# Kernel optimization log

Measured on AMD Instinct MI355X. Metric: run time of the kernel, lower is better.

Reference implementation:

```python
import jax, jax.numpy as jnp
import numpy as np
from jax import lax

T, B = 32, 16
NUM_ACTIONS = 18
HID = 256
C_V, C_K, C_S, NQ = 120, 8, 64, 4
NKEY, NVAL = C_K + C_S, C_V + C_S
Hh, Ww = 27, 20


def _spatial_basis():
    # Fourier spatial basis from Mott et al.; U = V = 8 -> 64 channels.
    h, w, U = Hh, Ww, 8
    p_h = np.arange(1, h + 1)[:, None] * np.ones((1, w)) * (np.pi / h)
    p_w = np.ones((h, 1)) * np.arange(1, w + 1)[None, :] * (np.pi / w)
    u = np.arange(1, U + 1)
    a = np.cos(p_h[:, :, None] * u)  # (h,w,8)
    b = np.cos(p_w[:, :, None] * u)  # (h,w,8)
    S = np.einsum('hwu,hwv->hwuv', a, b).reshape(h, w, U * U)
    return jnp.asarray(S, jnp.float32)

_S = _spatial_basis()


def _conv(x, w, b, stride, pad):
    y = lax.conv_general_dilated(x, w, stride, pad,
                                 dimension_numbers=('NCHW', 'OIHW', 'NCHW'))
    return y + b[None, :, None, None]


def setup_inputs() -> dict:
    key = jax.random.key(0)
    ks = iter(jax.random.split(key, 40))
    f32 = jnp.float32
    def rn(shape, s=0.05):
        return jax.random.normal(next(ks), shape, dtype=f32) * s
    return dict(
        frame=jax.random.normal(next(ks), (T, B, 3, 210, 160), dtype=f32),
        done=jnp.zeros((T, B), dtype=bool),
        last_action=jax.random.randint(next(ks), (T, B), 0, NUM_ACTIONS),
        reward=jax.random.normal(next(ks), (T, B), dtype=f32),
        core_h=jnp.zeros((B, HID), f32), core_c=jnp.zeros((B, HID), f32),
        conv_h=jnp.zeros((B, HID // 2, Hh, Ww), f32),
        conv_c=jnp.zeros((B, HID // 2, Hh, Ww), f32),
        cnn_w1=rn((32, 3, 8, 8)), cnn_b1=rn((32,)),
        cnn_w2=rn((64, 32, 4, 4)), cnn_b2=rn((64,)),
        lstm_w=rn((512, 192, 3, 3)), lstm_b=rn((512,)),
        qw1=rn((HID, 128)), qb1=rn((128,)),
        qw2=rn((128, NQ * NKEY)), qb2=rn((NQ * NKEY,)),
        qw3=rn((NQ * NKEY, NQ * NKEY)), qb3=rn((NQ * NKEY,)),
        aw1=rn((NVAL * NQ + NKEY * NQ + 1 + NUM_ACTIONS, 2 * HID)), ab1=rn((2 * HID,)),
        aw2=rn((2 * HID, HID)), ab2=rn((HID,)),
        w_ih=rn((4 * HID, HID)), w_hh=rn((4 * HID, HID)),
        b_ih=rn((4 * HID,)), b_hh=rn((4 * HID,)),
        pw=rn((HID, NUM_ACTIONS)), pb=rn((NUM_ACTIONS,)),
        vw=rn((HID, 1)), vb=rn((1,)),
    )


def reference(frame, done, last_action, reward, core_h, core_c, conv_h, conv_c,
              cnn_w1, cnn_b1, cnn_w2, cnn_b2, lstm_w, lstm_b,
              qw1, qb1, qw2, qb2, qw3, qb3, aw1, ab1, aw2, ab2,
              w_ih, w_hh, b_ih, b_hh, pw, pb, vw, vb):
    x = frame.reshape(T * B, 3, 210, 160)
    x = _conv(x, cnn_w1, cnn_b1, (4, 4), [(1, 1), (2, 2)])
    x = _conv(x, cnn_w2, cnn_b2, (2, 2), [(2, 2), (1, 1)])  # (T*B,64,27,20)
    x = x.reshape(T, B, 64, Hh, Ww)
    nd = (~done).astype(jnp.float32)  # (T,B)

    def vis_step(carry, inp):
        h, c = carry
        x_t, nd_t = inp
        m = nd_t[:, None, None, None]
        h, c = m * h, m * c
        gates = _conv(jnp.concatenate([x_t, h], axis=1), lstm_w, lstm_b,
                      (1, 1), [(1, 1), (1, 1)])
        ai, af, ao, ag = jnp.split(gates, 4, axis=1)
        c = jax.nn.sigmoid(af) * c + jax.nn.sigmoid(ai) * jnp.tanh(ag)
        h = jax.nn.sigmoid(ao) * jnp.tanh(c)
        return (h, c), h

    (vh, vc), O = lax.scan(vis_step, (conv_h, conv_c), (x, nd))
    # Faithful to the original `.view(N, h, w, c)` (a reinterpret, not a transpose).
    O = O.reshape(T * B, Hh, Ww, 128)
    Sb = jnp.broadcast_to(_S, (T * B, Hh, Ww, C_S))
    K = jnp.concatenate([O[..., :C_K], Sb], axis=3).reshape(T, B, Hh, Ww, NKEY)
    V = jnp.concatenate([O[..., C_K:], Sb], axis=3).reshape(T, B, Hh, Ww, NVAL)

    a1h = jax.nn.one_hot(last_action, NUM_ACTIONS, dtype=jnp.float32)  # (T,B,A)
    r = jnp.clip(reward, -1.0, 1.0)[..., None]  # (T,B,1)

    def core_step(carry, inp):
        h, c = carry
        K_t, V_t, r_t, a_t, nd_t = inp
        q = jax.nn.relu(h @ qw1 + qb1)
        q = jax.nn.relu(q @ qw2 + qb2)
        q = (q @ qw3 + qb3).reshape(B, NQ, NKEY)
        A = jnp.einsum('bhwk,bqk->bhwq', K_t, q)
        A = jax.nn.softmax(A.reshape(B, Hh * Ww, NQ), axis=1).reshape(B, Hh, Ww, NQ)
        ans = jnp.einsum('bhwq,bhwv->bqv', A, V_t)  # (B,NQ,NVAL)
        answer = jnp.concatenate(
            [ans.reshape(B, -1), q.reshape(B, -1), r_t, a_t], axis=1)
        ci = jax.nn.relu(answer @ aw1 + ab1) @ aw2 + ab2
        m = nd_t[:, None]
        h, c = m * h, m * c
        gates = ci @ w_ih.T + b_ih + h @ w_hh.T + b_hh  # torch gate order i,f,g,o
        gi, gf, gg, go = jnp.split(gates, 4, axis=1)
        c = jax.nn.sigmoid(gf) * c + jax.nn.sigmoid(gi) * jnp.tanh(gg)
        h = jax.nn.sigmoid(go) * jnp.tanh(c)
        return (h, c), h

    (ch, cc), outs = lax.scan(core_step, (core_h, core_c), (K, V, r, a1h, nd))
    out = outs.reshape(T * B, HID)
    logits = out @ pw + pb
    values = out @ vw + vb
    action = jnp.argmax(logits, axis=1)  # eval-mode action selection
    return (logits.reshape(T, B, NUM_ACTIONS), values.reshape(T, B),
            action.reshape(T, B), ch, cc, vh, vc)
```

## Files before the change

### kernel.cpp

```cpp
#include <hip/hip_runtime.h>
#include <math.h>

#define T_ 32
#define B_ 16
#define NA 18
#define P_ 540

typedef __attribute__((ext_vector_type(8)))  short short8;
typedef __attribute__((ext_vector_type(16))) float f32x16;

__device__ __forceinline__ float sigm(float x){ return 1.0f/(1.0f+expf(-x)); }
__device__ __forceinline__ unsigned short f2bf(float f){
    unsigned u = __float_as_uint(f);
    u += 0x7fff + ((u>>16)&1u);
    return (unsigned short)(u>>16);
}
__device__ __forceinline__ float bfu(unsigned short u){ return __uint_as_float(((unsigned)u)<<16); }

__global__ __launch_bounds__(256) void conv1k(const float* __restrict__ frame,
                                              const float* __restrict__ w,
                                              const float* __restrict__ bias,
                                              unsigned short* __restrict__ c1pad){
    __shared__ float tile[6048];
    int bid = blockIdx.x;
    int n = bid / 26, oh = (bid % 26)*2;
    int tid = threadIdx.x;
    const float* fb = frame + (size_t)n*3*210*160;
    for (int s = tid; s < 6048; s += 256){
        int col = s % 168;
        int row = (s/168) % 12;
        int ic  = s / 2016;
        int iy = oh*4 - 1 + row;
        int ix = col - 2;
        float v = 0.f;
        if (iy >= 0 && iy < 210 && ix >= 0 && ix < 160) v = fb[ic*33600 + iy*160 + ix];
        tile[s] = v;
    }
    __syncthreads();
    int oc = tid & 31, grp = tid >> 5;
    float acc[10] = {0.f,0.f,0.f,0.f,0.f,0.f,0.f,0.f,0.f,0.f};
    const float* wb = w + oc*192;
    for (int ic=0; ic<3; ++ic){
        #pragma unroll
        for (int kh=0; kh<8; ++kh){
            const float* wr = wb + ic*64 + kh*8;
            float4 w0 = *((const float4*)wr);
            float4 w1 = *((const float4*)(wr+4));
            const float* rowA = tile + ic*2016 + kh*168 + grp*20;
            float r[24];
            *((float4*)(r+ 0)) = *((const float4*)(rowA+ 0));
            *((float4*)(r+ 4)) = *((const float4*)(rowA+ 4));
            *((float4*)(r+ 8)) = *((const float4*)(rowA+ 8));
            *((float4*)(r+12)) = *((const float4*)(rowA+12));
            *((float4*)(r+16)) = *((const float4*)(rowA+16));
            *((float4*)(r+20)) = *((const float4*)(rowA+20));
            #pragma unroll
            for (int o=0;o<5;++o){
                acc[o] += r[o*4+0]*w0.x + r[o*4+1]*w0.y + r[o*4+2]*w0.z + r[o*4+3]*w0.w
                        + r[o*4+4]*w1.x + r[o*4+5]*w1.y + r[o*4+6]*w1.z + r[o*4+7]*w1.w;
            }
            const float* rowB = rowA + 672;
            *((float4*)(r+ 0)) = *((const float4*)(rowB+ 0));
            *((float4*)(r+ 4)) = *((const float4*)(rowB+ 4));
            *((float4*)(r+ 8)) = *((const float4*)(rowB+ 8));
            *((float4*)(r+12)) = *((const float4*)(rowB+12));
            *((float4*)(r+16)) = *((const float4*)(rowB+16));
            *((float4*)(r+20)) = *((const float4*)(rowB+20));
            #pragma unroll
            for (int o=0;o<5;++o){
                acc[5+o] += r[o*4+0]*w0.x + r[o*4+1]*w0.y + r[o*4+2]*w0.z + r[o*4+3]*w0.w
                          + r[o*4+4]*w1.x + r[o*4+5]*w1.y + r[o*4+6]*w1.z + r[o*4+7]*w1.w;
            }
        }
    }
    float bi = bias[oc];
    unsigned short* ob = c1pad + ((size_t)(n*32 + oc)*56 + oh+2)*42 + 1;
    #pragma unroll
    for (int o=0;o<5;++o) ob[grp*5+o] = f2bf(acc[o] + bi);
    ob += 42;
    #pragma unroll
    for (int o=0;o<5;++o) ob[grp*5+o] = f2bf(acc[5+o] + bi);
}

__global__ void apack2k(const float* __restrict__ w2, unsigned short* __restrict__ ap){
    int idx = blockIdx.x*256 + threadIdx.x;
    if (idx >= 32768) return;
    int j = idx & 7;
    int lane = (idx>>3) & 63;
    int mt = (idx>>9) & 1;
    int ic = idx >> 10;
    int k = ((lane>>5)<<3) + j;
    int oc = mt*32 + (lane & 31);
    ap[idx] = f2bf(w2[((oc*32 + ic)<<4) + k]);
}

__global__ __launch_bounds__(256) void c2mfma(const unsigned short* __restrict__ c1pad,
                                              const unsigned short* __restrict__ apack2,
                                              const float* __restrict__ bias,
                                              unsigned short* __restrict__ xre){
    __shared__ unsigned short p2[2][3072];
    __shared__ float bsm[64];
    int bid = blockIdx.x;
    int s = bid / 5;
    int n0 = (bid % 5) * 128;
    int tid = threadIdx.x;
    int wave = tid >> 6, lane = tid & 63;
    int khalf = (lane>>5) << 3;
    if (tid < 64) bsm[tid] = bias[tid];
    const unsigned short* cb = c1pad + (size_t)s*32*2352;

    int soff[8], swaddr[8];
    #pragma unroll
    for (int q=0;q<8;++q){
        int idx = q*256 + tid;
        int n = idx & 127, k = idx >> 7;
        int p = n0 + n; if (p > 539) p = 539;
        soff[q] = ((p/20)*2 + (k>>2))*42 + (p%20)*2 + (k&3);
        swaddr[q] = n*24 + k;
    }
    #pragma unroll
    for (int q=0;q<8;++q) p2[0][swaddr[q]] = cb[soff[q]];
    unsigned short rv[8];
    #pragma unroll
    for (int q=0;q<8;++q) rv[q] = cb[2352 + soff[q]];

    int mt = wave >> 1, ntb = (wave & 1) * 2;
    short8 acur = *((const short8*)(apack2 + ((size_t)mt*64 + lane)*8));
    short8 anxt;
    f32x16 acc[2];
    #pragma unroll
    for (int jj=0;jj<2;++jj)
        #pragma unroll
        for (int rg=0;rg<16;++rg) acc[jj][rg] = 0.f;
    __syncthreads();

    for (int c=0; c<32; ++c){
        int buf = c & 1;
        if (c < 31){
            #pragma unroll
            for (int q=0;q<8;++q) p2[buf^1][swaddr[q]] = rv[q];
        }
        if (c < 30){
            const unsigned short* src = cb + (size_t)(c+2)*2352;
            #pragma unroll
            for (int q=0;q<8;++q) rv[q] = src[soff[q]];
        }
        if (c < 31) anxt = *((const short8*)(apack2 + ((size_t)((c+1)*2 + mt)*64 + lane)*8));
        #pragma unroll
        for (int jj=0;jj<2;++jj){
            int n = (ntb+jj)*32 + (lane & 31);
            short8 bf = *((const short8*)(&p2[buf][n*24 + khalf]));
            acc[jj] = __builtin_amdgcn_mfma_f32_32x32x16_bf16(acur, bf, acc[jj], 0, 0, 0);
        }
        acur = anxt;
        __syncthreads();
    }
    #pragma unroll
    for (int jj=0;jj<2;++jj){
        int pos = n0 + (ntb+jj)*32 + (lane & 31);
        if (pos >= 540) continue;
        unsigned short* op = xre + ((size_t)s*540 + pos)*64;
        #pragma unroll
        for (int rg=0; rg<16; ++rg){
            int oc = mt*32 + (rg & 3) + 8*(rg>>2) + 4*(lane>>5);
            op[oc] = f2bf(acc[jj][rg] + bsm[oc]);
        }
    }
}

__global__ void sbasisk(float* __restrict__ S){
    int idx = blockIdx.x*256 + threadIdx.x;
    if (idx >= P_*64) return;
    int s = idx & 63, p = idx >> 6;
    int y = p/20, x = p%20;
    int u = s >> 3, v = s & 7;
    double a  = cos((double)((y+1)*(u+1)) * M_PI / 27.0);
    double bb = cos((double)((x+1)*(v+1)) * M_PI / 20.0);
    S[idx] = (float)(a*bb);
}

__global__ void packw4k(const float* __restrict__ in, unsigned short* __restrict__ out, int R, int C){
    int idx = blockIdx.x*256 + threadIdx.x;
    int r4cnt = (R+3)>>2;
    if (idx >= r4cnt*C*4) return;
    int j = idx & 3;
    int rc = idx >> 2;
    int c = rc % C;
    int r = (rc / C)*4 + j;
    out[idx] = (r < R) ? f2bf(in[(size_t)r*C + c]) : (unsigned short)0;
}
__global__ void packt4k(const float* __restrict__ in, unsigned short* __restrict__ out, int R, int C){
    int idx = blockIdx.x*256 + threadIdx.x;
    int r4cnt = (R+3)>>2;
    if (idx >= r4cnt*C*4) return;
    int j = idx & 3;
    int rc = idx >> 2;
    int c = rc % C;
    int r = (rc / C)*4 + j;
    out[idx] = (r < R) ? f2bf(in[(size_t)c*R + r]) : (unsigned short)0;
}

__global__ void apack9k(const float* __restrict__ lw, unsigned short* __restrict__ ap){
    int idx = blockIdx.x*256 + threadIdx.x;
    if (idx >= 884736) return;
    int j = idx & 7;
    int lane = (idx>>3) & 63;
    int mt = (idx>>9) & 15;
    int f  = idx >> 13;
    int tap = f / 12, c = f % 12;
    int ch = c*16 + ((lane>>5)<<3) + j;
    int oc = mt*32 + (lane & 31);
    ap[idx] = f2bf(lw[(size_t)oc*1728 + ch*9 + tap]);
}

__global__ void h0rek(const float* __restrict__ h0, unsigned short* __restrict__ h0re){
    int idx = blockIdx.x*256 + threadIdx.x;
    if (idx >= 16*128*540) return;
    int plane = idx / 540, p = idx % 540;
    int b = plane >> 7, c = plane & 127;
    h0re[((size_t)b*540 + p)*128 + c] = f2bf(h0[idx]);
}

__global__ __launch_bounds__(512) void gvck(const unsigned short* __restrict__ xre,
                                            const unsigned short* __restrict__ hrd,
                                            unsigned short* __restrict__ hwr,
                                            const unsigned short* __restrict__ h0re,
                                            const unsigned short* __restrict__ apack,
                                            const float* __restrict__ lb,
                                            const unsigned char* __restrict__ done,
                                            float* __restrict__ vh, float* __restrict__ vc,
                                            unsigned short* __restrict__ hreA,
                                            const float* __restrict__ S,
                                            const unsigned short* __restrict__ pq1, const float* __restrict__ qb1,
                                            const unsigned short* __restrict__ pq2, const float* __restrict__ qb2,
                                            const unsigned short* __restrict__ pq3, const float* __restrict__ qb3,
                                            const unsigned short* __restrict__ pa1, const float* __restrict__ ab1,
                                            const unsigned short* __restrict__ pa2, const float* __restrict__ ab2,
                                            const unsigned short* __restrict__ pih, const unsigned short* __restrict__ phh,
                                            const float* __restrict__ bih, const float* __restrict__ bhh,
                                            const float* __restrict__ reward, const int* __restrict__ lact,
                                            float* __restrict__ hsb, float* __restrict__ csb,
                                            float* __restrict__ outs,
                                            int t){
    __shared__ __align__(16) unsigned char smraw[65536];
    int bid = blockIdx.x;
    int tid = threadIdx.x;

    if (bid >= 16){
        if (t >= T_) return;
        float* gsm = (float*)smraw;
        int vb = bid - 16;
        int b  = vb % 16;
        int r  = vb / 16;
        int nb = r % 9;
        int mh = r / 9;
        int wave = tid >> 6, lane = tid & 63;
        int khalf = (lane>>5) << 3;
        int n0 = nb * 64;
        bool dn = done[t*B_ + b];

        const unsigned short* xb = xre + (size_t)(t*B_ + b)*540*64;
        const unsigned short* hp2 = (t==0) ? (h0re + (size_t)b*540*128)
                                           : (hrd  + (size_t)b*540*128);

        int mt = (wave>>1)*4 + mh*2 + (wave&1);

        int poff[2][9]; int vmask[2][9];
        #pragma unroll
        for (int jj=0;jj<2;++jj){
            int p = n0 + jj*32 + (lane & 31); if (p > 539) p = 539;
            int y = p/20, x = p%20;
            #pragma unroll
            for (int tap=0;tap<9;++tap){
                int dy = tap/3 - 1, dx = tap%3 - 1;
                int yy = y+dy, xx = x+dx;
                vmask[jj][tap] = ((unsigned)yy < 27u) && ((unsigned)xx < 20u);
                poff[jj][tap] = yy*20 + xx;
            }
        }
// ... 66 lines not shown
                    int pos = (flat/2560)*20 + (flat/128)%20;
                    int ch  = flat & 127;
                    hreA[((size_t)(t*B_ + b)*540 + pos)*128 + ch] = hb16;
                }
            }
        }
        return;
    }

    if (t == 0) return;
    int tc = t - 1;
    int b = bid;
    float* fs = (float*)smraw;
    float* hs   = fs;
    float* cs   = fs + 256;
    float* hs2  = fs + 512;
    float* q1   = fs + 768;
    float* q2   = fs + 896;
    float* q3   = fs + 1184;
    float* elog = fs + 1472;
    float* red  = fs + 3632;
    float* ansv = fs + 3664;
    float* hid  = fs + 4720;
    float* cis  = fs + 5232;
    float* gb   = fs + 5488;

    if (tid < 256){ hs[tid] = hsb[b*256+tid]; cs[tid] = csb[b*256+tid]; }
    if (tid >= 256 && tid < 269) ansv[1043 + (tid-256)] = 0.f;
    __syncthreads();

    float m = done[tc*B_+b] ? 0.f : 1.f;
    if (tid < 128){
        float a0=0.f,a1=0.f,a2=0.f,a3=0.f;
        for (int i4=0;i4<64;++i4){
            ushort4 w = *((const ushort4*)(pq1 + (size_t)((i4<<7)+tid)*4));
            float4 h4 = *((const float4*)(hs + i4*4));
            a0 += h4.x*bfu(w.x); a1 += h4.y*bfu(w.y);
            a2 += h4.z*bfu(w.z); a3 += h4.w*bfu(w.w);
        }
        q1[tid] = fmaxf(qb1[tid] + ((a0+a1)+(a2+a3)), 0.f);
    }
    __syncthreads();
    if (tid < 288){
        float a0=0.f,a1=0.f,a2=0.f,a3=0.f;
        for (int i4=0;i4<32;++i4){
            ushort4 w = *((const ushort4*)(pq2 + (size_t)(i4*288+tid)*4));
            float4 h4 = *((const float4*)(q1 + i4*4));
            a0 += h4.x*bfu(w.x); a1 += h4.y*bfu(w.y);
            a2 += h4.z*bfu(w.z); a3 += h4.w*bfu(w.w);
        }
        q2[tid] = fmaxf(qb2[tid] + ((a0+a1)+(a2+a3)), 0.f);
    }
    __syncthreads();
    if (tid < 288){
        float a0=0.f,a1=0.f,a2=0.f,a3=0.f;
        for (int i4=0;i4<72;++i4){
            ushort4 w = *((const ushort4*)(pq3 + (size_t)(i4*288+tid)*4));
            float4 h4 = *((const float4*)(q2 + i4*4));
            a0 += h4.x*bfu(w.x); a1 += h4.y*bfu(w.y);
            a2 += h4.z*bfu(w.z); a3 += h4.w*bfu(w.w);
        }
        float a = qb3[tid] + ((a0+a1)+(a2+a3));
        q3[tid] = a;
        ansv[736+tid] = a;
    }
    if (tid == 0){ float r = reward[tc*B_+b]; ansv[1024] = fminf(1.f,fmaxf(-1.f,r)); }
    if (tid >= 32 && tid < 32+NA) ansv[1025 + tid-32] = (lact[tc*B_+b] == tid-32) ? 1.f : 0.f;
    __syncthreads();

    const unsigned short* hrb = hreA + (size_t)(tc*B_ + b)*540*128;
    for (int idx = tid; idx < 4*P_; idx += 512){
        int qi = idx / P_, p = idx % P_;
        const unsigned short* hp = hrb + (size_t)p*128;
        uint4 hv = *((const uint4*)hp);
        const float* qv = q3 + qi*72;
        float a = __uint_as_float(hv.x<<16)*qv[0] + __uint_as_float(hv.x & 0xffff0000u)*qv[1]
                + __uint_as_float(hv.y<<16)*qv[2] + __uint_as_float(hv.y & 0xffff0000u)*qv[3]
                + __uint_as_float(hv.z<<16)*qv[4] + __uint_as_float(hv.z & 0xffff0000u)*qv[5]
                + __uint_as_float(hv.w<<16)*qv[6] + __uint_as_float(hv.w & 0xffff0000u)*qv[7];
        const float* Sp = S + p*64;
        #pragma unroll
        for (int s2=0;s2<16;++s2){
            float4 sv = *((const float4*)(Sp + 4*s2));
            a += sv.x*qv[8+4*s2] + sv.y*qv[9+4*s2] + sv.z*qv[10+4*s2] + sv.w*qv[11+4*s2];
        }
        elog[qi*P_ + p] = a;
    }
    __syncthreads();
    {
        int qi = tid >> 7, lt = tid & 127;
        float mx = -1e30f;
        for (int p = lt; p < P_; p += 128) mx = fmaxf(mx, elog[qi*P_ + p]);
        for (int off=32; off; off>>=1) mx = fmaxf(mx, __shfl_down(mx, off));
        if ((tid & 63) == 0) red[tid>>6] = mx;
        __syncthreads();
        if (tid < 4) red[16+tid] = fmaxf(red[2*tid], red[2*tid+1]);
        __syncthreads();
        mx = red[16+qi];
        float sm = 0.f;
        for (int p = lt; p < P_; p += 128){ float e = expf(elog[qi*P_ + p]-mx); elog[qi*P_ + p] = e; sm += e; }
        for (int off=32; off; off>>=1) sm += __shfl_down(sm, off);
        if ((tid & 63) == 0) red[8 + (tid>>6)] = sm;
        __syncthreads();
        if (tid < 4) red[24+tid] = red[8+2*tid] + red[8+2*tid+1];
        __syncthreads();
    }
    if (tid < 240){
        int g = tid >> 2;
        int qi = g / 15, vb = g % 15;
        int pc = tid & 3;
        float ac[8] = {0,0,0,0,0,0,0,0};
        const unsigned short* hb8 = hrb + 8 + vb*8;
        for (int p = pc*135; p < pc*135+135; ++p){
            float e = elog[qi*P_ + p];
            uint4 hv = *((const uint4*)(hb8 + (size_t)p*128));
            ac[0] += e*__uint_as_float(hv.x<<16);
            ac[1] += e*__uint_as_float(hv.x & 0xffff0000u);
            ac[2] += e*__uint_as_float(hv.y<<16);
            ac[3] += e*__uint_as_float(hv.y & 0xffff0000u);
            ac[4] += e*__uint_as_float(hv.z<<16);
            ac[5] += e*__uint_as_float(hv.z & 0xffff0000u);
            ac[6] += e*__uint_as_float(hv.w<<16);
            ac[7] += e*__uint_as_float(hv.w & 0xffff0000u);
        }
        #pragma unroll
        for (int j=0;j<8;++j){ ac[j] += __shfl_down(ac[j],2); ac[j] += __shfl_down(ac[j],1); }
        if ((tid&3)==0){
            float inv2 = 1.f/red[24+qi];
            #pragma unroll
            for (int j=0;j<8;++j) ansv[qi*184 + vb*8 + j] = ac[j]*inv2;
        }
    } else if (tid < 496){
        int u = tid - 240;
        int g = u >> 2;
        int qi = g >> 4, vb4 = g & 15;
        int pc = u & 3;
        float ac[4] = {0,0,0,0};
        const float* Sp = S + vb4*4;
        for (int p = pc*135; p < pc*135+135; ++p){
            float e = elog[qi*P_ + p];
            float4 sv = *((const float4*)(Sp + (size_t)p*64));
            ac[0]+=e*sv.x; ac[1]+=e*sv.y; ac[2]+=e*sv.z; ac[3]+=e*sv.w;
        }
        #pragma unroll
        for (int j=0;j<4;++j){ ac[j] += __shfl_down(ac[j],2); ac[j] += __shfl_down(ac[j],1); }
        if ((tid&3)==0){
            float inv2 = 1.f/red[24+qi];
            #pragma unroll
            for (int j=0;j<4;++j) ansv[qi*184 + 120 + vb4*4 + j] = ac[j]*inv2;
        }
    }
    __syncthreads();
    {
        float a0=ab1[tid], a1=0.f, a2=0.f, a3=0.f;
        for (int i4=0;i4<261;++i4){
            ushort4 w = *((const ushort4*)(pa1 + (size_t)((i4<<9)+tid)*4));
            float4 av = *((const float4*)(ansv + i4*4));
            a0 += av.x*bfu(w.x); a1 += av.y*bfu(w.y);
            a2 += av.z*bfu(w.z); a3 += av.w*bfu(w.w);
        }
        hid[tid] = fmaxf((a0+a1)+(a2+a3), 0.f);
    }
    if (tid < 256) hs2[tid] = hs[tid]*m;
    __syncthreads();
    if (tid < 256){
        float a0=ab2[tid],a1=0.f,a2=0.f,a3=0.f;
        for (int i4=0;i4<128;++i4){
            ushort4 w = *((const ushort4*)(pa2 + (size_t)((i4<<8)+tid)*4));
            float4 hv = *((const float4*)(hid + i4*4));
            a0 += hv.x*bfu(w.x); a1 += hv.y*bfu(w.y);
            a2 += hv.z*bfu(w.z); a3 += hv.w*bfu(w.w);
        }
        cis[tid] = (a0+a1)+(a2+a3);
    }
    __syncthreads();
    for (int g = tid; g < 1024; g += 512){
        float a0=bih[g]+bhh[g], a1=0.f, a2=0.f, a3=0.f;
        for (int i4=0;i4<64;++i4){
            ushort4 wi = *((const ushort4*)(pih + (size_t)((i4<<10)+g)*4));
            ushort4 wh = *((const ushort4*)(phh + (size_t)((i4<<10)+g)*4));
            float4 cv = *((const float4*)(cis + i4*4));
            float4 hv = *((const float4*)(hs2 + i4*4));
            a0 += cv.x*bfu(wi.x) + hv.x*bfu(wh.x);
            a1 += cv.y*bfu(wi.y) + hv.y*bfu(wh.y);
            a2 += cv.z*bfu(wi.z) + hv.z*bfu(wh.z);
            a3 += cv.w*bfu(wi.w) + hv.w*bfu(wh.w);
        }
        gb[g] = (a0+a1)+(a2+a3);
    }
    __syncthreads();
    if (tid < 256){
        float gi = gb[tid], gf = gb[256+tid], gg = gb[512+tid], go = gb[768+tid];
        float cold = cs[tid]*m;
        float cn = sigm(gf)*cold + sigm(gi)*tanhf(gg);
        float hn = sigm(go)*tanhf(cn);
        csb[b*256+tid] = cn;
        hsb[b*256+tid] = hn;
        outs[(tc*B_+b)*256+tid] = hn;
    }
}

__global__ __launch_bounds__(64) void finalk(const float* __restrict__ outs,
                                             const float* __restrict__ pw, const float* __restrict__ pb,
                                             const float* __restrict__ vw, const float* __restrict__ vb,
                                             float* __restrict__ dout){
    int row = blockIdx.x, tid = threadIdx.x;
    __shared__ float os[256];
    __shared__ float lg[NA];
    for (int i=tid; i<256; i+=64) os[i] = outs[row*256+i];
    __syncthreads();
    if (tid < NA){
        float a = pb[tid];
        for (int i=0;i<256;++i) a += os[i]*pw[i*NA+tid];
        lg[tid] = a;
        dout[row*NA + tid] = a;
    } else if (tid == 32){
        float a = vb[0];
        for (int i=0;i<256;++i) a += os[i]*vw[i];
        dout[9216 + row] = a;
// ... 7 lines not shown
}

extern "C" void kernel_launch(void* const* d_in, const int* in_sizes, int n_in,
                              void* d_out, int out_size, void* d_ws, size_t ws_size,
                              hipStream_t stream) {
    const float* frame   = (const float*)d_in[0];
    const unsigned char* done = (const unsigned char*)d_in[1];
    const int*   lact    = (const int*)d_in[2];
    const float* reward  = (const float*)d_in[3];
    const float* core_h0 = (const float*)d_in[4];
    const float* core_c0 = (const float*)d_in[5];
    const float* conv_h0 = (const float*)d_in[6];
    const float* conv_c0 = (const float*)d_in[7];
    const float* cnn_w1  = (const float*)d_in[8];
    const float* cnn_b1  = (const float*)d_in[9];
    const float* cnn_w2  = (const float*)d_in[10];
    const float* cnn_b2  = (const float*)d_in[11];
    const float* lstm_w  = (const float*)d_in[12];
    const float* lstm_b  = (const float*)d_in[13];
    const float* qw1 = (const float*)d_in[14]; const float* qb1 = (const float*)d_in[15];
    const float* qw2 = (const float*)d_in[16]; const float* qb2 = (const float*)d_in[17];
    const float* qw3 = (const float*)d_in[18]; const float* qb3 = (const float*)d_in[19];
    const float* aw1 = (const float*)d_in[20]; const float* ab1 = (const float*)d_in[21];
    const float* aw2 = (const float*)d_in[22]; const float* ab2 = (const float*)d_in[23];
    const float* w_ih = (const float*)d_in[24]; const float* w_hh = (const float*)d_in[25];
    const float* b_ih = (const float*)d_in[26]; const float* b_hh = (const float*)d_in[27];
    const float* pw = (const float*)d_in[28]; const float* pb = (const float*)d_in[29];
    const float* vw = (const float*)d_in[30]; const float* vb = (const float*)d_in[31];

    float* ws = (float*)d_ws;
    float* dout = (float*)d_out;

    unsigned short* xre    = (unsigned short*)ws;
    unsigned short* c1pad  = (unsigned short*)(ws + 10485760);
    unsigned short* hreA   = (unsigned short*)(ws + 10485760);
    unsigned short* apack  = (unsigned short*)(ws + 28180480);
    unsigned short* wpk    = (unsigned short*)(ws + 28966912);
    unsigned short* pq1 = wpk;
    unsigned short* pq2 = wpk + 32768;
    unsigned short* pq3 = wpk + 69632;
    unsigned short* pa1 = wpk + 152576;
    unsigned short* pa2 = wpk + 687104;
    unsigned short* pih = wpk + 818176;
    unsigned short* phh = wpk + 1080320;
    unsigned short* h0re   = (unsigned short*)(ws + 29753344);
    unsigned short* apack2 = (unsigned short*)(ws + 30408704);
    unsigned short* hpl0   = (unsigned short*)(ws + 30425088);
    float* hsb   = ws + 31080448;
    float* csb   = ws + 31084544;
    unsigned short* hpl1   = (unsigned short*)(ws + 31100928);
    float* vh    = ws + 34881536;
    float* vc    = ws + 35987456;
    float* S     = ws + 37093376;
    float* outs  = ws + 37127936;

    hipMemsetAsync(c1pad, 0, (size_t)38535168*2, stream);

    apack2k<<<128, 256, 0, stream>>>(cnn_w2, apack2);
    conv1k<<<512*26, 256, 0, stream>>>(frame, cnn_w1, cnn_b1, c1pad);
    c2mfma<<<2560, 256, 0, stream>>>(c1pad, apack2, cnn_b2, xre);

    sbasisk<<<135, 256, 0, stream>>>(S);
    apack9k<<<3456, 256, 0, stream>>>(lstm_w, apack);
    packw4k<<<128,  256, 0, stream>>>(qw1, pq1, 256, 128);
    packw4k<<<144,  256, 0, stream>>>(qw2, pq2, 128, 288);
    packw4k<<<324,  256, 0, stream>>>(qw3, pq3, 288, 288);
    packw4k<<<2088, 256, 0, stream>>>(aw1, pa1, 1043, 512);
    packw4k<<<512,  256, 0, stream>>>(aw2, pa2, 512, 256);
    packt4k<<<1024, 256, 0, stream>>>(w_ih, pih, 256, 1024);
    packt4k<<<1024, 256, 0, stream>>>(w_hh, phh, 256, 1024);
    h0rek<<<4320, 256, 0, stream>>>(conv_h0, h0re);
    hipMemcpyAsync(vc,  conv_c0, (size_t)16*128*540*sizeof(float), hipMemcpyDeviceToDevice, stream);
    hipMemcpyAsync(hsb, core_h0, (size_t)16*256*sizeof(float), hipMemcpyDeviceToDevice, stream);
    hipMemcpyAsync(csb, core_c0, (size_t)16*256*sizeof(float), hipMemcpyDeviceToDevice, stream);

    for (int t = 0; t <= T_; ++t){
        gvck<<<304, 512, 0, stream>>>(xre,
                                      (t&1)?hpl0:hpl1, (t&1)?hpl1:hpl0, h0re,
                                      apack, lstm_b, done, vh, vc, hreA,
                                      S, pq1,qb1,pq2,qb2,pq3,qb3,
                                      pa1,ab1,pa2,ab2, pih,phh,b_ih,b_hh,
                                      reward, lact, hsb, csb, outs, t);
    }

    finalk<<<512, 64, 0, stream>>>(outs, pw, pb, vw, vb, dout);

    hipMemcpyAsync(dout + 10240,   outs + (size_t)31*B_*256, (size_t)16*256*sizeof(float), hipMemcpyDeviceToDevice, stream);
    hipMemcpyAsync(dout + 14336,   csb, (size_t)16*256*sizeof(float), hipMemcpyDeviceToDevice, stream);
    hipMemcpyAsync(dout + 18432,   vh,  (size_t)16*128*540*sizeof(float), hipMemcpyDeviceToDevice, stream);
    hipMemcpyAsync(dout + 1124352, vc,  (size_t)16*128*540*sizeof(float), hipMemcpyDeviceToDevice, stream);
}
```

Measured before the change: 4.801 ms.

## Overlap CNN encoder with recurrent steps inside the per-timestep kernel

The conv1 and conv2 stages no longer run over all frames up front. A prologue computes timesteps 0 and 1, and each per-timestep gvck launch gets extra blocks that compute conv1 for t+2 and conv2 for t+1 into a 3-slot ring buffer. This hides encoder work behind the latency-bound recurrent steps and shrinks the c1 buffer. The change also widens the bf16 weight packing from 4 to 8 elements per vector load in the FC layers and adds a transposed spatial basis for a strided reduction. The risk is that the extra blocks compete with the recurrent blocks for CUs, and the ring-slot indexing and padding must stay correct.

```diff
diff --git a/kernel.cpp b/kernel.cpp
--- a/kernel.cpp
+++ b/kernel.cpp
@@ -16,17 +16,17 @@
     return (unsigned short)(u>>16);
 }
 __device__ __forceinline__ float bfu(unsigned short u){ return __uint_as_float(((unsigned)u)<<16); }
-
-__global__ __launch_bounds__(256) void conv1k(const float* __restrict__ frame,
-                                              const float* __restrict__ w,
-                                              const float* __restrict__ bias,
-                                              unsigned short* __restrict__ c1pad){
-    __shared__ float tile[6048];
-    int bid = blockIdx.x;
-    int n = bid / 26, oh = (bid % 26)*2;
-    int tid = threadIdx.x;
+__device__ __forceinline__ float BFLO(unsigned x){ return __uint_as_float(x<<16); }
+__device__ __forceinline__ float BFHI(unsigned x){ return __uint_as_float(x & 0xffff0000u); }
+
+__device__ __forceinline__ void conv1_block(const float* __restrict__ frame,
+                                            const float* __restrict__ w,
+                                            const float* __restrict__ bias,
+                                            unsigned short* __restrict__ c1buf,
+                                            int n, int slot, int oh, int tid, char* smraw){
+    float* tile = (float*)smraw;
     const float* fb = frame + (size_t)n*3*210*160;
-    for (int s = tid; s < 6048; s += 256){
+    for (int s = tid; s < 6048; s += 512){
         int col = s % 168;
         int row = (s/168) % 12;
         int ic  = s / 2016;
@@ -37,8 +37,8 @@
         tile[s] = v;
     }
     __syncthreads();
-    int oc = tid & 31, grp = tid >> 5;
-    float acc[10] = {0.f,0.f,0.f,0.f,0.f,0.f,0.f,0.f,0.f,0.f};
+    int oc = tid & 31, grp = (tid >> 5) & 7, rsel = tid >> 8;
+    float acc[5] = {0.f,0.f,0.f,0.f,0.f};
     const float* wb = w + oc*192;
     for (int ic=0; ic<3; ++ic){
         #pragma unroll
@@ -46,40 +46,107 @@
             const float* wr = wb + ic*64 + kh*8;
             float4 w0 = *((const float4*)wr);
             float4 w1 = *((const float4*)(wr+4));
-            const float* rowA = tile + ic*2016 + kh*168 + grp*20;
+            const float* row = tile + ic*2016 + (kh + 4*rsel)*168 + grp*20;
             float r[24];
-            *((float4*)(r+ 0)) = *((const float4*)(rowA+ 0));
-            *((float4*)(r+ 4)) = *((const float4*)(rowA+ 4));
-            *((float4*)(r+ 8)) = *((const float4*)(rowA+ 8));
-            *((float4*)(r+12)) = *((const float4*)(rowA+12));
-            *((float4*)(r+16)) = *((const float4*)(rowA+16));
-            *((float4*)(r+20)) = *((const float4*)(rowA+20));
+            *((float4*)(r+ 0)) = *((const float4*)(row+ 0));
+            *((float4*)(r+ 4)) = *((const float4*)(row+ 4));
+            *((float4*)(r+ 8)) = *((const float4*)(row+ 8));
+            *((float4*)(r+12)) = *((const float4*)(row+12));
+            *((float4*)(r+16)) = *((const float4*)(row+16));
+            *((float4*)(r+20)) = *((const float4*)(row+20));
             #pragma unroll
             for (int o=0;o<5;++o){
                 acc[o] += r[o*4+0]*w0.x + r[o*4+1]*w0.y + r[o*4+2]*w0.z + r[o*4+3]*w0.w
                         + r[o*4+4]*w1.x + r[o*4+5]*w1.y + r[o*4+6]*w1.z + r[o*4+7]*w1.w;
             }
-            const float* rowB = rowA + 672;
-            *((float4*)(r+ 0)) = *((const float4*)(rowB+ 0));
-            *((float4*)(r+ 4)) = *((const float4*)(rowB+ 4));
-            *((float4*)(r+ 8)) = *((const float4*)(rowB+ 8));
-            *((float4*)(r+12)) = *((const float4*)(rowB+12));
-            *((float4*)(r+16)) = *((const float4*)(rowB+16));
-            *((float4*)(r+20)) = *((const float4*)(rowB+20));
-            #pragma unroll
-            for (int o=0;o<5;++o){
-                acc[5+o] += r[o*4+0]*w0.x + r[o*4+1]*w0.y + r[o*4+2]*w0.z + r[o*4+3]*w0.w
-                          + r[o*4+4]*w1.x + r[o*4+5]*w1.y + r[o*4+6]*w1.z + r[o*4+7]*w1.w;
-            }
         }
     }
     float bi = bias[oc];
-    unsigned short* ob = c1pad + ((size_t)(n*32 + oc)*56 + oh+2)*42 + 1;
+    unsigned short* ob = c1buf + ((size_t)((slot*16 + (n & 15))*32 + oc)*56 + oh+2+rsel)*42 + 1;
     #pragma unroll
     for (int o=0;o<5;++o) ob[grp*5+o] = f2bf(acc[o] + bi);
-    ob += 42;
+}
+
+__device__ __forceinline__ void c2_block(const unsigned short* __restrict__ c1buf,
+                                         const unsigned short* __restrict__ apack2,
+                                         const float* __restrict__ bias,
+                                         unsigned short* __restrict__ xre,
+                                         int s, int slot, int n0, int tid, char* smraw){
+    unsigned short (*p2)[3072] = (unsigned short (*)[3072])smraw;
+    float* bsm = (float*)(smraw + 12288);
+    int wave = tid >> 6, lane = tid & 63;
+    int khalf = (lane>>5) << 3;
+    if (tid < 64) bsm[tid] = bias[tid];
+    const unsigned short* cb = c1buf + (size_t)(slot*16 + (s & 15))*32*2352;
+
+    int soff[4], swaddr[4];
     #pragma unroll
-    for (int o=0;o<5;++o) ob[grp*5+o] = f2bf(acc[5+o] + bi);
+    for (int q=0;q<4;++q){
+        int idx = q*512 + tid;
+        int n = idx & 127, k = idx >> 7;
+        int p = n0 + n; if (p > 539) p = 539;
+        soff[q] = ((p/20)*2 + (k>>2))*42 + (p%20)*2 + (k&3);
+        swaddr[q] = n*24 + k;
+    }
+    #pragma unroll
+    for (int q=0;q<4;++q) p2[0][swaddr[q]] = cb[soff[q]];
+    unsigned short rv[4];
+    #pragma unroll
+    for (int q=0;q<4;++q) rv[q] = cb[2352 + soff[q]];
+
+    int mt = wave >> 2, nq = wave & 3;
+    short8 acur = *((const short8*)(apack2 + ((size_t)mt*64 + lane)*8));
+    short8 anxt;
+    f32x16 acc;
+    #pragma unroll
+    for (int rg=0;rg<16;++rg) acc[rg] = 0.f;
+    __syncthreads();
+
+    for (int c=0; c<32; ++c){
+        int buf = c & 1;
+        if (c < 31){
+            #pragma unroll
+            for (int q=0;q<4;++q) p2[buf^1][swaddr[q]] = rv[q];
+        }
+        if (c < 30){
+            const unsigned short* src = cb + (size_t)(c+2)*2352;
+            #pragma unroll
+            for (int q=0;q<4;++q) rv[q] = src[soff[q]];
+        }
+        if (c < 31) anxt = *((const short8*)(apack2 + ((size_t)((c+1)*2 + mt)*64 + lane)*8));
+        {
+            int n = nq*32 + (lane & 31);
+            short8 bf = *((const short8*)(&p2[buf][n*24 + khalf]));
+            acc = __builtin_amdgcn_mfma_f32_32x32x16_bf16(acur, bf, acc, 0, 0, 0);
+        }
+        acur = anxt;
+        __syncthreads();
+    }
+    int pos = n0 + nq*32 + (lane & 31);
+    if (pos < 540){
+        unsigned short* op = xre + ((size_t)s*540 + pos)*64;
+        #pragma unroll
+        for (int rg=0; rg<16; ++rg){
+            int oc = mt*32 + (rg & 3) + 8*(rg>>2) + 4*(lane>>5);
+            op[oc] = f2bf(acc[rg] + bsm[oc]);
+        }
+    }
+}
+
+__global__ __launch_bounds__(512) void conv1pro(const float* __restrict__ frame,
+                                                const float* __restrict__ w,
+                                                const float* __restrict__ bias,
+                                                unsigned short* __restrict__ c1buf){
+    __shared__ __align__(16) char sm[24576];
+    int n = blockIdx.x/26, oh = (blockIdx.x%26)*2;
+    conv1_block(frame, w, bias, c1buf, n, (n>>4)%3, oh, threadIdx.x, sm);
+}
+__global__ __launch_bounds__(512) void c2pro(const unsigned short* __restrict__ c1buf,
+                                             const unsigned short* __restrict__ apack2,
+                                             const float* __restrict__ bias,
+                                             unsigned short* __restrict__ xre){
+    __shared__ __align__(16) char sm[12544];
+    c2_block(c1buf, apack2, bias, xre, blockIdx.x/5, 0, (blockIdx.x%5)*128, threadIdx.x, sm);
 }
 
 __global__ void apack2k(const float* __restrict__ w2, unsigned short* __restrict__ ap){
@@ -94,81 +161,7 @@
     ap[idx] = f2bf(w2[((oc*32 + ic)<<4) + k]);
 }
 
-__global__ __launch_bounds__(256) void c2mfma(const unsigned short* __restrict__ c1pad,
-                                              const unsigned short* __restrict__ apack2,
-                                              const float* __restrict__ bias,
-                                              unsigned short* __restrict__ xre){
-    __shared__ unsigned short p2[2][3072];
-    __shared__ float bsm[64];
-    int bid = blockIdx.x;
-    int s = bid / 5;
-    int n0 = (bid % 5) * 128;
-    int tid = threadIdx.x;
-    int wave = tid >> 6, lane = tid & 63;
-    int khalf = (lane>>5) << 3;
-    if (tid < 64) bsm[tid] = bias[tid];
-    const unsigned short* cb = c1pad + (size_t)s*32*2352;
-
-    int soff[8], swaddr[8];
-    #pragma unroll
-    for (int q=0;q<8;++q){
-        int idx = q*256 + tid;
-        int n = idx & 127, k = idx >> 7;
-        int p = n0 + n; if (p > 539) p = 539;
-        soff[q] = ((p/20)*2 + (k>>2))*42 + (p%20)*2 + (k&3);
-        swaddr[q] = n*24 + k;
-    }
-    #pragma unroll
-    for (int q=0;q<8;++q) p2[0][swaddr[q]] = cb[soff[q]];
-    unsigned short rv[8];
-    #pragma unroll
-    for (int q=0;q<8;++q) rv[q] = cb[2352 + soff[q]];
-
-    int mt = wave >> 1, ntb = (wave & 1) * 2;
-    short8 acur = *((const short8*)(apack2 + ((size_t)mt*64 + lane)*8));
-    short8 anxt;
-    f32x16 acc[2];
-    #pragma unroll
-    for (int jj=0;jj<2;++jj)
-        #pragma unroll
-        for (int rg=0;rg<16;++rg) acc[jj][rg] = 0.f;
-    __syncthreads();
-
-    for (int c=0; c<32; ++c){
-        int buf = c & 1;
-        if (c < 31){
-            #pragma unroll
-            for (int q=0;q<8;++q) p2[buf^1][swaddr[q]] = rv[q];
-        }
-        if (c < 30){
-            const unsigned short* src = cb + (size_t)(c+2)*2352;
-            #pragma unroll
-            for (int q=0;q<8;++q) rv[q] = src[soff[q]];
-        }
-        if (c < 31) anxt = *((const short8*)(apack2 + ((size_t)((c+1)*2 + mt)*64 + lane)*8));
-        #pragma unroll
-        for (int jj=0;jj<2;++jj){
-            int n = (ntb+jj)*32 + (lane & 31);
-            short8 bf = *((const short8*)(&p2[buf][n*24 + khalf]));
-            acc[jj] = __builtin_amdgcn_mfma_f32_32x32x16_bf16(acur, bf, acc[jj], 0, 0, 0);
-        }
-        acur = anxt;
-        __syncthreads();
-    }
-    #pragma unroll
-    for (int jj=0;jj<2;++jj){
-        int pos = n0 + (ntb+jj)*32 + (lane & 31);
-        if (pos >= 540) continue;
-        unsigned short* op = xre + ((size_t)s*540 + pos)*64;
-        #pragma unroll
-        for (int rg=0; rg<16; ++rg){
-            int oc = mt*32 + (rg & 3) + 8*(rg>>2) + 4*(lane>>5);
-            op[oc] = f2bf(acc[jj][rg] + bsm[oc]);
-        }
-    }
-}
-
-__global__ void sbasisk(float* __restrict__ S){
+__global__ void sbasisk(float* __restrict__ S, float* __restrict__ ST){
     int idx = blockIdx.x*256 + threadIdx.x;
     if (idx >= P_*64) return;
     int s = idx & 63, p = idx >> 6;
@@ -176,27 +169,29 @@
     int u = s >> 3, v = s & 7;
     double a  = cos((double)((y+1)*(u+1)) * M_PI / 27.0);
     double bb = cos((double)((x+1)*(v+1)) * M_PI / 20.0);
-    S[idx] = (float)(a*bb);
-}
-
-__global__ void packw4k(const float* __restrict__ in, unsigned short* __restrict__ out, int R, int C){
+    float fv = (float)(a*bb);
+    S[idx] = fv;
+    ST[(size_t)s*540 + p] = fv;
+}
+
+__global__ void packw8k(const float* __restrict__ in, unsigned short* __restrict__ out, int R, int C){
     int idx = blockIdx.x*256 + threadIdx.x;
-    int r4cnt = (R+3)>>2;
-    if (idx >= r4cnt*C*4) return;
-    int j = idx & 3;
-    int rc = idx >> 2;
+    int r8cnt = (R+7)>>3;
+    if (idx >= r8cnt*C*8) return;
+    int j = idx & 7;
+    int rc = idx >> 3;
     int c = rc % C;
-    int r = (rc / C)*4 + j;
+    int r = (rc / C)*8 + j;
     out[idx] = (r < R) ? f2bf(in[(size_t)r*C + c]) : (unsigned short)0;
 }
-__global__ void packt4k(const float* __restrict__ in, unsigned short* __restrict__ out, int R, int C){
+__global__ void packt8k(const float* __restrict__ in, unsigned short* __restrict__ out, int R, int C){
     int idx = blockIdx.x*256 + threadIdx.x;
-    int r4cnt = (R+3)>>2;
-    if (idx >= r4cnt*C*4) return;
-    int j = idx & 3;
-    int rc = idx >> 2;
+    int r8cnt = (R+7)>>3;
+    if (idx >= r8cnt*C*8) return;
+    int j = idx & 7;
+    int rc = idx >> 3;
     int c = rc % C;
-    int r = (rc / C)*4 + j;
+    int r = (rc / C)*8 + j;
     out[idx] = (r < R) ? f2bf(in[(size_t)c*R + r]) : (unsigned short)0;
 }
 
@@ -221,7 +216,13 @@
     h0re[((size_t)b*540 + p)*128 + c] = f2bf(h0[idx]);
 }
 
-__global__ __launch_bounds__(512) void gvck(const unsigned short* __restrict__ xre,
+__global__ __launch_bounds__(512) void gvck(const float* __restrict__ frame,
+                                            const float* __restrict__ cnn_w1,
+                                            const float* __restrict__ cnn_b1,
+                                            unsigned short* __restrict__ c1buf,
+                                            const unsigned short* __restrict__ apack2,
+                                            const float* __restrict__ cnn_b2,
+                                            unsigned short* __restrict__ xre,
                                             const unsigned short* __restrict__ hrd,
                                             unsigned short* __restrict__ hwr,
                                             const unsigned short* __restrict__ h0re,
@@ -231,6 +232,7 @@
                                             float* __restrict__ vh, float* __restrict__ vc,
                                             unsigned short* __restrict__ hreA,
                                             const float* __restrict__ S,
+                                            const float* __restrict__ ST,
                                             const unsigned short* __restrict__ pq1, const float* __restrict__ qb1,
                                             const unsigned short* __restrict__ pq2, const float* __restrict__ qb2,
                                             const unsigned short* __restrict__ pq3, const float* __restrict__ qb3,
@@ -242,9 +244,22 @@
                                             float* __restrict__ hsb, float* __restrict__ csb,
                                             float* __restrict__ outs,
                                             int t){
-    __shared__ __align__(16) unsigned char smraw[65536];
+    __shared__ __align__(16) char smraw[65536];
     int bid = blockIdx.x;
     int tid = threadIdx.x;
+
+    if (bid >= 720){
+        int tp1 = t + 1; if (tp1 > 31) return;
+        int idx = bid - 720;
+        c2_block(c1buf, apack2, cnn_b2, xre, tp1*16 + idx/5, tp1%3, (idx%5)*128, tid, smraw);
+        return;
+    }
+    if (bid >= 304){
+        int tp2 = t + 2; if (tp2 > 31) return;
+        int idx = bid - 304;
+        conv1_block(frame, cnn_w1, cnn_b1, c1buf, tp2*16 + idx/26, tp2%3, (idx%26)*2, tid, smraw);
+        return;
+    }
 
     if (bid >= 16){
         if (t >= T_) return;
@@ -377,33 +392,42 @@
     float m = done[tc*B_+b] ? 0.f : 1.f;
     if (tid < 128){
         float a0=0.f,a1=0.f,a2=0.f,a3=0.f;
-        for (int i4=0;i4<64;++i4){
-            ushort4 w = *((const ushort4*)(pq1 + (size_t)((i4<<7)+tid)*4));
-            float4 h4 = *((const float4*)(hs + i4*4));
-            a0 += h4.x*bfu(w.x); a1 += h4.y*bfu(w.y);
-            a2 += h4.z*bfu(w.z); a3 += h4.w*bfu(w.w);
+        for (int i8=0;i8<32;++i8){
+            uint4 w = *((const uint4*)(pq1 + ((size_t)(i8<<7)+tid)*8));
+            float4 ha = *((const float4*)(hs + i8*8));
+            float4 hb2 = *((const float4*)(hs + i8*8 + 4));
+            a0 += ha.x*BFLO(w.x);  a1 += ha.y*BFHI(w.x);
+            a2 += ha.z*BFLO(w.y);  a3 += ha.w*BFHI(w.y);
+            a0 += hb2.x*BFLO(w.z); a1 += hb2.y*BFHI(w.z);
+            a2 += hb2.z*BFLO(w.w); a3 += hb2.w*BFHI(w.w);
         }
         q1[tid] = fmaxf(qb1[tid] + ((a0+a1)+(a2+a3)), 0.f);
     }
     __syncthreads();
     if (tid < 288){
         float a0=0.f,a1=0.f,a2=0.f,a3=0.f;
-        for (int i4=0;i4<32;++i4){
-            ushort4 w = *((const ushort4*)(pq2 + (size_t)(i4*288+tid)*4));
-            float4 h4 = *((const float4*)(q1 + i4*4));
-            a0 += h4.x*bfu(w.x); a1 += h4.y*bfu(w.y);
-            a2 += h4.z*bfu(w.z); a3 += h4.w*bfu(w.w);
+        for (int i8=0;i8<16;++i8){
+            uint4 w = *((const uint4*)(pq2 + ((size_t)i8*288+tid)*8));
+            float4 ha = *((const float4*)(q1 + i8*8));
+            float4 hb2 = *((const float4*)(q1 + i8*8 + 4));
+            a0 += ha.x*BFLO(w.x);  a1 += ha.y*BFHI(w.x);
+            a2 += ha.z*BFLO(w.y);  a3 += ha.w*BFHI(w.y);
+            a0 += hb2.x*BFLO(w.z); a1 += hb2.y*BFHI(w.z);
+            a2 += hb2.z*BFLO(w.w); a3 += hb2.w*BFHI(w.w);
         }
         q2[tid] = fmaxf(qb2[tid] + ((a0+a1)+(a2+a3)), 0.f);
     }
     __syncthreads();
     if (tid < 288){
         float a0=0.f,a1=0.f,a2=0.f,a3=0.f;
-        for (int i4=0;i4<72;++i4){
-            ushort4 w = *((const ushort4*)(pq3 + (size_t)(i4*288+tid)*4));
-            float4 h4 = *((const float4*)(q2 + i4*4));
-            a0 += h4.x*bfu(w.x); a1 += h4.y*bfu(w.y);
-            a2 += h4.z*bfu(w.z); a3 += h4.w*bfu(w.w);
+        for (int i8=0;i8<36;++i8){
+            uint4 w = *((const uint4*)(pq3 + ((size_t)i8*288+tid)*8));
+            float4 ha = *((const float4*)(q2 + i8*8));
+            float4 hb2 = *((const float4*)(q2 + i8*8 + 4));
+            a0 += ha.x*BFLO(w.x);  a1 += ha.y*BFHI(w.x);
+            a2 += ha.z*BFLO(w.y);  a3 += ha.w*BFHI(w.y);
+            a0 += hb2.x*BFLO(w.z); a1 += hb2.y*BFHI(w.z);
+            a2 += hb2.z*BFLO(w.w); a3 += hb2.w*BFHI(w.w);
         }
         float a = qb3[tid] + ((a0+a1)+(a2+a3));
         q3[tid] = a;
@@ -419,10 +443,10 @@
         const unsigned short* hp = hrb + (size_t)p*128;
         uint4 hv = *((const uint4*)hp);
         const float* qv = q3 + qi*72;
-        float a = __uint_as_float(hv.x<<16)*qv[0] + __uint_as_float(hv.x & 0xffff0000u)*qv[1]
-                + __uint_as_float(hv.y<<16)*qv[2] + __uint_as_float(hv.y & 0xffff0000u)*qv[3]
-                + __uint_as_float(hv.z<<16)*qv[4] + __uint_as_float(hv.z & 0xffff0000u)*qv[5]
-                + __uint_as_float(hv.w<<16)*qv[6] + __uint_as_float(hv.w & 0xffff0000u)*qv[7];
+        float a = BFLO(hv.x)*qv[0] + BFHI(hv.x)*qv[1]
+                + BFLO(hv.y)*qv[2] + BFHI(hv.y)*qv[3]
+                + BFLO(hv.z)*qv[4] + BFHI(hv.z)*qv[5]
+                + BFLO(hv.w)*qv[6] + BFHI(hv.w)*qv[7];
         const float* Sp = S + p*64;
         #pragma unroll
         for (int s2=0;s2<16;++s2){
@@ -450,59 +474,61 @@
         if (tid < 4) red[24+tid] = red[8+2*tid] + red[8+2*tid+1];
         __syncthreads();
     }
-    if (tid < 240){
-        int g = tid >> 2;
+    if (tid < 480){
+        int g = tid >> 3;
         int qi = g / 15, vb = g % 15;
-        int pc = tid & 3;
+        int pc = tid & 7;
         float ac[8] = {0,0,0,0,0,0,0,0};
         const unsigned short* hb8 = hrb + 8 + vb*8;
-        for (int p = pc*135; p < pc*135+135; ++p){
+        for (int p = pc; p < P_; p += 8){
             float e = elog[qi*P_ + p];
             uint4 hv = *((const uint4*)(hb8 + (size_t)p*128));
-            ac[0] += e*__uint_as_float(hv.x<<16);
-            ac[1] += e*__uint_as_float(hv.x & 0xffff0000u);
-            ac[2] += e*__uint_as_float(hv.y<<16);
-            ac[3] += e*__uint_as_float(hv.y & 0xffff0000u);
-            ac[4] += e*__uint_as_float(hv.z<<16);
-            ac[5] += e*__uint_as_float(hv.z & 0xffff0000u);
-            ac[6] += e*__uint_as_float(hv.w<<16);
-            ac[7] += e*__uint_as_float(hv.w & 0xffff0000u);
+            ac[0] += e*BFLO(hv.x); ac[1] += e*BFHI(hv.x);
+            ac[2] += e*BFLO(hv.y); ac[3] += e*BFHI(hv.y);
+            ac[4] += e*BFLO(hv.z); ac[5] += e*BFHI(hv.z);
+            ac[6] += e*BFLO(hv.w); ac[7] += e*BFHI(hv.w);
         }
         #pragma unroll
-        for (int j=0;j<8;++j){ ac[j] += __shfl_down(ac[j],2); ac[j] += __shfl_down(ac[j],1); }
-        if ((tid&3)==0){
+        for (int j=0;j<8;++j){ ac[j] += __shfl_down(ac[j],4); ac[j] += __shfl_down(ac[j],2); ac[j] += __shfl_down(ac[j],1); }
+        if (pc == 0){
             float inv2 = 1.f/red[24+qi];
             #pragma unroll
             for (int j=0;j<8;++j) ansv[qi*184 + vb*8 + j] = ac[j]*inv2;
         }
-    } else if (tid < 496){
-        int u = tid - 240;
-        int g = u >> 2;
+    }
+    {
+        int g = tid >> 3;
         int qi = g >> 4, vb4 = g & 15;
-        int pc = u & 3;
-        float ac[4] = {0,0,0,0};
-        const float* Sp = S + vb4*4;
-        for (int p = pc*135; p < pc*135+135; ++p){
+        int pc = tid & 7;
+        float s0=0.f, s1=0.f, s2v=0.f, s3=0.f;
+        const float* S0 = ST + (size_t)(vb4*4)*540;
+        for (int p = pc; p < P_; p += 8){
             float e = elog[qi*P_ + p];
-            float4 sv = *((const float4*)(Sp + (size_t)p*64));
-            ac[0]+=e*sv.x; ac[1]+=e*sv.y; ac[2]+=e*sv.z; ac[3]+=e*sv.w;
-        }
-        #pragma unroll
-        for (int j=0;j<4;++j){ ac[j] += __shfl_down(ac[j],2); ac[j] += __shfl_down(ac[j],1); }
-        if ((tid&3)==0){
+            s0 += e*S0[p]; s1 += e*S0[540+p]; s2v += e*S0[1080+p]; s3 += e*S0[1620+p];
+        }
+        s0 += __shfl_down(s0,4); s0 += __shfl_down(s0,2); s0 += __shfl_down(s0,1);
+        s1 += __shfl_down(s1,4); s1 += __shfl_down(s1,2); s1 += __shfl_down(s1,1);
+        s2v += __shfl_down(s2v,4); s2v += __shfl_down(s2v,2); s2v += __shfl_down(s2v,1);
+        s3 += __shfl_down(s3,4); s3 += __shfl_down(s3,2); s3 += __shfl_down(s3,1);
+        if (pc == 0){
             float inv2 = 1.f/red[24+qi];
-            #pragma unroll
-            for (int j=0;j<4;++j) ansv[qi*184 + 120 + vb4*4 + j] = ac[j]*inv2;
+            ansv[qi*184 + 120 + vb4*4 + 0] = s0*inv2;
+            ansv[qi*184 + 120 + vb4*4 + 1] = s1*inv2;
+            ansv[qi*184 + 120 + vb4*4 + 2] = s2v*inv2;
+            ansv[qi*184 + 120 + vb4*4 + 3] = s3*inv2;
         }
     }
     __syncthreads();
     {
         float a0=ab1[tid], a1=0.f, a2=0.f, a3=0.f;
-        for (int i4=0;i4<261;++i4){
-            ushort4 w = *((const ushort4*)(pa1 + (size_t)((i4<<9)+tid)*4));
-            float4 av = *((const float4*)(ansv + i4*4));
-            a0 += av.x*bfu(w.x); a1 += av.y*bfu(w.y);
-            a2 += av.z*bfu(w.z); a3 += av.w*bfu(w.w);
+        for (int i8=0;i8<131;++i8){
+            uint4 w = *((const uint4*)(pa1 + ((size_t)(i8<<9)+tid)*8));
+            float4 av = *((const float4*)(ansv + i8*8));
+            float4 av2 = *((const float4*)(ansv + i8*8 + 4));
+            a0 += av.x*BFLO(w.x);  a1 += av.y*BFHI(w.x);
+            a2 += av.z*BFLO(w.y);  a3 += av.w*BFHI(w.y);
+            a0 += av2.x*BFLO(w.z); a1 += av2.y*BFHI(w.z);
+            a2 += av2.z*BFLO(w.w); a3 += av2.w*BFHI(w.w);
         }
         hid[tid] = fmaxf((a0+a1)+(a2+a3), 0.f);
     }
@@ -510,26 +536,35 @@
     __syncthreads();
     if (tid < 256){
         float a0=ab2[tid],a1=0.f,a2=0.f,a3=0.f;
-        for (int i4=0;i4<128;++i4){
-            ushort4 w = *((const ushort4*)(pa2 + (size_t)((i4<<8)+tid)*4));
-            float4 hv = *((const float4*)(hid + i4*4));
-            a0 += hv.x*bfu(w.x); a1 += hv.y*bfu(w.y);
-            a2 += hv.z*bfu(w.z); a3 += hv.w*bfu(w.w);
+        for (int i8=0;i8<64;++i8){
+            uint4 w = *((const uint4*)(pa2 + ((size_t)(i8<<8)+tid)*8));
+            float4 hv = *((const float4*)(hid + i8*8));
+            float4 hv2 = *((const float4*)(hid + i8*8 + 4));
+            a0 += hv.x*BFLO(w.x);  a1 += hv.y*BFHI(w.x);
+            a2 += hv.z*BFLO(w.y);  a3 += hv.w*BFHI(w.y);
+            a0 += hv2.x*BFLO(w.z); a1 += hv2.y*BFHI(w.z);
+            a2 += hv2.z*BFLO(w.w); a3 += hv2.w*BFHI(w.w);
         }
         cis[tid] = (a0+a1)+(a2+a3);
     }
     __syncthreads();
     for (int g = tid; g < 1024; g += 512){
         float a0=bih[g]+bhh[g], a1=0.f, a2=0.f, a3=0.f;
-        for (int i4=0;i4<64;++i4){
-            ushort4 wi = *((const ushort4*)(pih + (size_t)((i4<<10)+g)*4));
-            ushort4 wh = *((const ushort4*)(phh + (size_t)((i4<<10)+g)*4));
-            float4 cv = *((const float4*)(cis + i4*4));
-            float4 hv = *((const float4*)(hs2 + i4*4));
-            a0 += cv.x*bfu(wi.x) + hv.x*bfu(wh.x);
-            a1 += cv.y*bfu(wi.y) + hv.y*bfu(wh.y);
-            a2 += cv.z*bfu(wi.z) + hv.z*bfu(wh.z);
-            a3 += cv.w*bfu(wi.w) + hv.w*bfu(wh.w);
+        for (int i8=0;i8<32;++i8){
+            uint4 wi = *((const uint4*)(pih + ((size_t)(i8<<10)+g)*8));
+            uint4 wh = *((const uint4*)(phh + ((size_t)(i8<<10)+g)*8));
+            float4 ca = *((const float4*)(cis + i8*8));
+            float4 cb2 = *((const float4*)(cis + i8*8 + 4));
+            float4 ha = *((const float4*)(hs2 + i8*8));
+            float4 hb2 = *((const float4*)(hs2 + i8*8 + 4));
+            a0 += ca.x*BFLO(wi.x) + ha.x*BFLO(wh.x);
+            a1 += ca.y*BFHI(wi.x) + ha.y*BFHI(wh.x);
+            a2 += ca.z*BFLO(wi.y) + ha.z*BFLO(wh.y);
+            a3 += ca.w*BFHI(wi.y) + ha.w*BFHI(wh.y);
+            a0 += cb2.x*BFLO(wi.z) + hb2.x*BFLO(wh.z);
+            a1 += cb2.y*BFHI(wi.z) + hb2.y*BFHI(wh.z);
+            a2 += cb2.z*BFLO(wi.w) + hb2.z*BFLO(wh.w);
+            a3 += cb2.w*BFHI(wi.w) + hb2.w*BFHI(wh.w);
         }
         gb[g] = (a0+a1)+(a2+a3);
     }
@@ -603,7 +638,6 @@
     float* dout = (float*)d_out;
 
     unsigned short* xre    = (unsigned short*)ws;
-    unsigned short* c1pad  = (unsigned short*)(ws + 10485760);
     unsigned short* hreA   = (unsigned short*)(ws + 10485760);
     unsigned short* apack  = (unsigned short*)(ws + 28180480);
     unsigned short* wpk    = (unsigned short*)(ws + 28966912);
@@ -611,45 +645,47 @@
     unsigned short* pq2 = wpk + 32768;
     unsigned short* pq3 = wpk + 69632;
     unsigned short* pa1 = wpk + 152576;
-    unsigned short* pa2 = wpk + 687104;
-    unsigned short* pih = wpk + 818176;
-    unsigned short* phh = wpk + 1080320;
+    unsigned short* pa2 = wpk + 689152;
+    unsigned short* pih = wpk + 820224;
+    unsigned short* phh = wpk + 1082368;
     unsigned short* h0re   = (unsigned short*)(ws + 29753344);
     unsigned short* apack2 = (unsigned short*)(ws + 30408704);
     unsigned short* hpl0   = (unsigned short*)(ws + 30425088);
     float* hsb   = ws + 31080448;
     float* csb   = ws + 31084544;
     unsigned short* hpl1   = (unsigned short*)(ws + 31100928);
+    unsigned short* c1buf  = (unsigned short*)(ws + 31653888);
+    float* ST    = ws + 33460224;
     float* vh    = ws + 34881536;
     float* vc    = ws + 35987456;
     float* S     = ws + 37093376;
     float* outs  = ws + 37127936;
 
-    hipMemsetAsync(c1pad, 0, (size_t)38535168*2, stream);
+    hipMemsetAsync(c1buf, 0, (size_t)3612672*2, stream);
 
     apack2k<<<128, 256, 0, stream>>>(cnn_w2, apack2);
-    conv1k<<<512*26, 256, 0, stream>>>(frame, cnn_w1, cnn_b1, c1pad);
-    c2mfma<<<2560, 256, 0, stream>>>(c1pad, apack2, cnn_b2, xre);
-
-    sbasisk<<<135, 256, 0, stream>>>(S);
+    sbasisk<<<135, 256, 0, stream>>>(S, ST);
     apack9k<<<3456, 256, 0, stream>>>(lstm_w, apack);
-    packw4k<<<128,  256, 0, stream>>>(qw1, pq1, 256, 128);
-    packw4k<<<144,  256, 0, stream>>>(qw2, pq2, 128, 288);
-    packw4k<<<324,  256, 0, stream>>>(qw3, pq3, 288, 288);
-    packw4k<<<2088, 256, 0, stream>>>(aw1, pa1, 1043, 512);
-    packw4k<<<512,  256, 0, stream>>>(aw2, pa2, 512, 256);
-    packt4k<<<1024, 256, 0, stream>>>(w_ih, pih, 256, 1024);
-    packt4k<<<1024, 256, 0, stream>>>(w_hh, phh, 256, 1024);
+    packw8k<<<128,  256, 0, stream>>>(qw1, pq1, 256, 128);
+    packw8k<<<144,  256, 0, stream>>>(qw2, pq2, 128, 288);
+    packw8k<<<324,  256, 0, stream>>>(qw3, pq3, 288, 288);
+    packw8k<<<2096, 256, 0, stream>>>(aw1, pa1, 1043, 512);
+    packw8k<<<512,  256, 0, stream>>>(aw2, pa2, 512, 256);
+    packt8k<<<1024, 256, 0, stream>>>(w_ih, pih, 256, 1024);
+    packt8k<<<1024, 256, 0, stream>>>(w_hh, phh, 256, 1024);
     h0rek<<<4320, 256, 0, stream>>>(conv_h0, h0re);
     hipMemcpyAsync(vc,  conv_c0, (size_t)16*128*540*sizeof(float), hipMemcpyDeviceToDevice, stream);
     hipMemcpyAsync(hsb, core_h0, (size_t)16*256*sizeof(float), hipMemcpyDeviceToDevice, stream);
     hipMemcpyAsync(csb, core_c0, (size_t)16*256*sizeof(float), hipMemcpyDeviceToDevice, stream);
 
+    conv1pro<<<832, 512, 0, stream>>>(frame, cnn_w1, cnn_b1, c1buf);
+    c2pro<<<80, 512, 0, stream>>>(c1buf, apack2, cnn_b2, xre);
+
     for (int t = 0; t <= T_; ++t){
-        gvck<<<304, 512, 0, stream>>>(xre,
+        gvck<<<800, 512, 0, stream>>>(frame, cnn_w1, cnn_b1, c1buf, apack2, cnn_b2, xre,
                                       (t&1)?hpl0:hpl1, (t&1)?hpl1:hpl0, h0re,
                                       apack, lstm_b, done, vh, vc, hreA,
-                                      S, pq1,qb1,pq2,qb2,pq3,qb3,
+                                      S, ST, pq1,qb1,pq2,qb2,pq3,qb3,
                                       pa1,ab1,pa2,ab2, pih,phh,b_ih,b_hh,
                                       reward, lact, hsb, csb, outs, t);
     }
```

Result: slower. 5.349 ms (+11.4%).
